# Optimization experiments

Hardware: AMD Instinct MI355X
Metric: run time of the kernel (lower is better)

Reference implementation:

```python
import math
import jax, jax.numpy as jnp
import numpy as np

B, T, C, H, E, K = 2, 2048, 1024, 16, 8, 2
HID = 4 * C
D = C // H

def new_gelu(x):
    return 0.5 * x * (1.0 + jnp.tanh(math.sqrt(2.0 / math.pi) * (x + 0.044715 * x ** 3)))

def layer_norm(x, g, b, eps=1e-5):
    mu = jnp.mean(x, axis=-1, keepdims=True)
    var = jnp.var(x, axis=-1, keepdims=True)
    return (x - mu) / jnp.sqrt(var + eps) * g + b

def setup_inputs():
    key = jax.random.key(0)
    ks = jax.random.split(key, 8)
    s = 0.02
    return {
        'x': jax.random.normal(ks[0], (B, T, C), jnp.float32),
        'ln1_g': jnp.ones((C,), jnp.float32), 'ln1_b': jnp.zeros((C,), jnp.float32),
        'ln2_g': jnp.ones((C,), jnp.float32), 'ln2_b': jnp.zeros((C,), jnp.float32),
        'attn_w': (jax.random.normal(ks[1], (C, 3 * C), jnp.float32) * s),
        'attn_b': jnp.zeros((3 * C,), jnp.float32),
        'proj_w': (jax.random.normal(ks[2], (C, C), jnp.float32) * s),
        'proj_b': jnp.zeros((C,), jnp.float32),
        'router_w': (jax.random.normal(ks[3], (C, E), jnp.float32) * s),
        'fc_w': (jax.random.normal(ks[4], (E, C, HID), jnp.float32) * s),
        'fc_b': jnp.zeros((E, HID), jnp.float32),
        'pj_w': (jax.random.normal(ks[5], (E, HID, C), jnp.float32) * s),
        'pj_b': jnp.zeros((E, C), jnp.float32),
    }

def reference(x, ln1_g, ln1_b, ln2_g, ln2_b, attn_w, attn_b, proj_w, proj_b, router_w, fc_w, fc_b, pj_w, pj_b):
    # --- causal self-attention with residual ---
    h = layer_norm(x, ln1_g, ln1_b)
    qkv = h @ attn_w + attn_b                              # [B,T,3C]
    q, k, v = jnp.split(qkv, 3, axis=-1)
    q = q.reshape(B, T, H, D).transpose(0, 2, 1, 3)        # [B,H,T,D]
    k = k.reshape(B, T, H, D).transpose(0, 2, 1, 3)
    v = v.reshape(B, T, H, D).transpose(0, 2, 1, 3)
    att = jnp.einsum('bhqd,bhkd->bhqk', q, k) * (1.0 / math.sqrt(D))
    mask = jnp.tril(jnp.ones((T, T), dtype=bool))
    att = jnp.where(mask, att, jnp.float32(-jnp.inf))
    att = jax.nn.softmax(att, axis=-1)                     # dropout p=0 (eval)
    y = jnp.einsum('bhqk,bhkd->bhqd', att, v)
    y = y.transpose(0, 2, 1, 3).reshape(B, T, C)
    x = x + (y @ proj_w + proj_b)
    # --- MoE FFN with residual ---
    h2 = layer_norm(x, ln2_g, ln2_b).reshape(B * T, C)     # [N,C]
    logits = h2 @ router_w                                 # [N,E]
    probs = jax.nn.softmax(logits, axis=-1)
    topk_p, topk_i = jax.lax.top_k(probs, K)               # [N,K]
    topk_p = topk_p / jnp.sum(topk_p, axis=-1, keepdims=True)
    # dense combine weights: zero outside selected experts (same math as scatter)
    gate = jnp.zeros((B * T, E), h2.dtype).at[jnp.arange(B * T)[:, None], topk_i].add(topk_p)
    out = jnp.zeros_like(h2)
    for e in range(E):  # fixed small expert loop
        he = new_gelu(h2 @ fc_w[e] + fc_b[e])              # [N,HID]
        out = out + gate[:, e:e + 1] * (he @ pj_w[e] + pj_b[e])
    return x + out.reshape(B, T, C)
```

## Files before the change

### kernel.cpp

```cpp
#include <hip/hip_runtime.h>
#include <math.h>


typedef __bf16 b16v8 __attribute__((ext_vector_type(8)));
typedef float f32x4 __attribute__((ext_vector_type(4)));

#define MFMA(a, b, c) __builtin_amdgcn_mfma_f32_16x16x32_bf16(a, b, c, 0, 0, 0)

#define GLOAD_LDS16(g, l)                                          \
  __builtin_amdgcn_global_load_lds(                                \
      (const __attribute__((address_space(1))) void*)(g),          \
      (__attribute__((address_space(3))) void*)(l), 16, 0, 0)

#define SYNC_VM0()                                       \
  do {                                                   \
    asm volatile("s_waitcnt vmcnt(0)" ::: "memory");     \
    __builtin_amdgcn_s_barrier();                        \
    asm volatile("" ::: "memory");                       \
  } while (0)

constexpr int Bc = 2, Tc = 2048, Cc = 1024, Hc = 16, Dc = 64;
constexpr int Nc = Bc * Tc;
constexpr int HIDc = 4096;
constexpr int Ec = 8;
constexpr int NPAIR = Nc * 2;
constexpr float LOG2E = 1.4426950408889634f;

__device__ inline unsigned short f32_bf16(float f) {
  union { float f; unsigned u; } x; x.f = f;
  unsigned r = x.u + 0x7fffu + ((x.u >> 16) & 1u);
  return (unsigned short)(r >> 16);
}

__device__ inline float gelu_f(float x) {
  float t = 2.3021188f * x * (1.f + 0.044715f * x * x);
  float e = __builtin_amdgcn_exp2f(-t);
  return x * __builtin_amdgcn_rcpf(1.f + e);
}

__global__ __launch_bounds__(256) void convT_kernel(
    const float* __restrict__ src, unsigned short* __restrict__ dst,
    int K, int N) {
  const size_t sb = (size_t)blockIdx.z * K * N;
  const int n0 = blockIdx.x * 32, k0 = blockIdx.y * 32;
  __shared__ float t[32][33];
  const int tx = threadIdx.x & 31, ty = threadIdx.x >> 5;
#pragma unroll
  for (int j = 0; j < 4; ++j)
    t[ty + j * 8][tx] = src[sb + (size_t)(k0 + ty + j * 8) * N + n0 + tx];
  __syncthreads();
#pragma unroll
  for (int j = 0; j < 4; ++j)
    dst[sb + (size_t)(n0 + ty + j * 8) * K + k0 + tx] = f32_bf16(t[tx][ty + j * 8]);
}

__global__ __launch_bounds__(256) void ln1_kernel(
    const float* __restrict__ x, const float* __restrict__ g,
    const float* __restrict__ b, unsigned short* __restrict__ out) {
  const int row = blockIdx.x;
  const int tid = threadIdx.x;
  const float* xr = x + (size_t)row * Cc;
  float v[4]; float s = 0.f, q = 0.f;
#pragma unroll
  for (int j = 0; j < 4; ++j) { v[j] = xr[tid + j * 256]; s += v[j]; q += v[j] * v[j]; }
#pragma unroll
  for (int m = 1; m <= 32; m <<= 1) { s += __shfl_xor(s, m); q += __shfl_xor(q, m); }
  __shared__ float red[2][4];
  const int w = tid >> 6;
  if ((tid & 63) == 0) { red[0][w] = s; red[1][w] = q; }
  __syncthreads();
  s = red[0][0] + red[0][1] + red[0][2] + red[0][3];
  q = red[1][0] + red[1][1] + red[1][2] + red[1][3];
  const float mean = s * (1.f / Cc);
  const float var = q * (1.f / Cc) - mean * mean;
  const float rstd = rsqrtf(var + 1e-5f);
#pragma unroll
  for (int j = 0; j < 4; ++j) {
    int c = tid + j * 256;
    out[(size_t)row * Cc + c] = f32_bf16((v[j] - mean) * rstd * g[c] + b[c]);
  }
}

__global__ __launch_bounds__(256) void ln2_router_kernel(
    const float* __restrict__ x, const float* __restrict__ g,
    const float* __restrict__ b, const float* __restrict__ rw,
    unsigned short* __restrict__ out, int* __restrict__ tki, float* __restrict__ tkp) {
  const int row = blockIdx.x;
  const int tid = threadIdx.x;
  const float* xr = x + (size_t)row * Cc;
  float v[4]; float s = 0.f, q = 0.f;
#pragma unroll
  for (int j = 0; j < 4; ++j) { v[j] = xr[tid + j * 256]; s += v[j]; q += v[j] * v[j]; }
#pragma unroll
  for (int m = 1; m <= 32; m <<= 1) { s += __shfl_xor(s, m); q += __shfl_xor(q, m); }
  __shared__ float red[2][4];
  const int w = tid >> 6;
  if ((tid & 63) == 0) { red[0][w] = s; red[1][w] = q; }
  __syncthreads();
  s = red[0][0] + red[0][1] + red[0][2] + red[0][3];
  q = red[1][0] + red[1][1] + red[1][2] + red[1][3];
  const float mean = s * (1.f / Cc);
  const float var = q * (1.f / Cc) - mean * mean;
  const float rstd = rsqrtf(var + 1e-5f);
  float lg[8] = {0.f, 0.f, 0.f, 0.f, 0.f, 0.f, 0.f, 0.f};
#pragma unroll
  for (int j = 0; j < 4; ++j) {
    int c = tid + j * 256;
    float nv = (v[j] - mean) * rstd * g[c] + b[c];
    out[(size_t)row * Cc + c] = f32_bf16(nv);
    const float* rwc = rw + c * 8;
#pragma unroll
    for (int e = 0; e < 8; ++e) lg[e] += nv * rwc[e];
  }
#pragma unroll
  for (int m = 1; m <= 32; m <<= 1) {
#pragma unroll
    for (int e = 0; e < 8; ++e) lg[e] += __shfl_xor(lg[e], m);
  }
  __shared__ float rl[4][8];
  if ((tid & 63) == 0) {
#pragma unroll
    for (int e = 0; e < 8; ++e) rl[w][e] = lg[e];
  }
  __syncthreads();
  if (tid == 0) {
    float L[8];
#pragma unroll
    for (int e = 0; e < 8; ++e) L[e] = rl[0][e] + rl[1][e] + rl[2][e] + rl[3][e];
    int i1 = 0;
    for (int e = 1; e < 8; ++e) if (L[e] > L[i1]) i1 = e;
    int i2 = (i1 == 0) ? 1 : 0;
    for (int e = 0; e < 8; ++e) if (e != i1 && L[e] > L[i2]) i2 = e;
    float e2 = expf(L[i2] - L[i1]);
    float inv = 1.f / (1.f + e2);
    tki[row * 2] = i1; tki[row * 2 + 1] = i2;
    tkp[row * 2] = inv; tkp[row * 2 + 1] = e2 * inv;
  }
}

__global__ __launch_bounds__(256) void count_kernel(
    const int* __restrict__ tki, int* __restrict__ counts) {
  int n = blockIdx.x * 256 + threadIdx.x;
  if (n >= Nc) return;
  atomicAdd(&counts[tki[n * 2]], 1);
  atomicAdd(&counts[tki[n * 2 + 1]], 1);
}

__global__ void scan_kernel(const int* __restrict__ counts,
                            int* __restrict__ eoff, int* __restrict__ cursor) {
  if (threadIdx.x == 0 && blockIdx.x == 0) {
    int s = 0;
    for (int e = 0; e < Ec; ++e) { eoff[e] = s; cursor[e] = s; s += counts[e]; }
    eoff[Ec] = s;
  }
}

__global__ __launch_bounds__(256) void assign_kernel(
    const int* __restrict__ tki, int* __restrict__ cursor,
    int* __restrict__ slot_tok, int* __restrict__ tok2slot) {
  int n = blockIdx.x * 256 + threadIdx.x;
  if (n >= Nc) return;
#pragma unroll
  for (int kk = 0; kk < 2; ++kk) {
    int e = tki[n * 2 + kk];
    int slot = atomicAdd(&cursor[e], 1);
    slot_tok[slot] = n;
    tok2slot[n * 2 + kk] = slot;
  }
}

struct GArgs {
  const unsigned short* A;
  const unsigned short* Bt;
  const float* bias;
  int M, N, K, lda;
  size_t Bstride; int biasStride;
  const int* eoff;
  const int* slot_tok;
  float* outF;
  const float* resid;
  unsigned short* outB;
  unsigned short* outK;
  unsigned short* outV;
};

template <int MODE>
__global__ __launch_bounds__(256) void gemm128(GArgs g) {
  const int e = blockIdx.z;
  int s0 = 0, Meff = g.M;
  if constexpr (MODE == 2 || MODE == 3) {
    s0 = g.eoff[e];
    Meff = g.eoff[e + 1] - s0;
  }
  const int row0 = blockIdx.y * 128;
  if (row0 >= Meff) return;
  const int col0 = blockIdx.x * 128;

  __shared__ __align__(16) unsigned short As[2][4096];
  __shared__ __align__(16) unsigned short Bs[2][4096];

  const int tid = threadIdx.x;
  const int lane = tid & 63, w = tid >> 6;
  const int wr = w >> 1, wc = w & 1;
  const int fr = lane & 15, fg = lane >> 4;

  const unsigned short* Bt = g.Bt + (size_t)e * g.Bstride;
  const float* bias = g.bias + (size_t)e * g.biasStride;

  size_t aaddr[2], baddr[2];
#pragma unroll
  for (int i = 0; i < 2; ++i) {
    int pos = i * 256 + tid;
    int r = pos >> 2, c8 = (pos & 3) * 8;
    int gr = row0 + r;
    if (gr >= Meff) gr = Meff - 1;
    int srcrow;
    if constexpr (MODE == 2) srcrow = g.slot_tok[s0 + gr];
    else if constexpr (MODE == 3) srcrow = s0 + gr;
    else srcrow = gr;
    aaddr[i] = (size_t)srcrow * g.lda + c8;
    baddr[i] = (size_t)(col0 + r) * g.K + c8;
  }

  auto STAGE = [&](int buf, int k0) {
#pragma unroll
    for (int i = 0; i < 2; ++i) {
      GLOAD_LDS16(g.A + aaddr[i] + k0, &As[buf][i * 2048 + w * 512]);
      GLOAD_LDS16(Bt + baddr[i] + k0, &Bs[buf][i * 2048 + w * 512]);
    }
  };

  f32x4 acc[4][4] = {};
  const int nt = g.K / 32;

  STAGE(0, 0);
  SYNC_VM0();
  int cur = 0;

  for (int t = 0; t < nt; ++t) {
    if (t + 1 < nt) STAGE(cur ^ 1, (t + 1) * 32);
    b16v8 af[4], bfr[4];
#pragma unroll
    for (int mi = 0; mi < 4; ++mi)
      af[mi] = *(const b16v8*)&As[cur][(wr * 64 + mi * 16 + fr) * 32 + fg * 8];
#pragma unroll
    for (int ni = 0; ni < 4; ++ni)
      bfr[ni] = *(const b16v8*)&Bs[cur][(wc * 64 + ni * 16 + fr) * 32 + fg * 8];
#pragma unroll
    for (int mi = 0; mi < 4; ++mi)
#pragma unroll
      for (int ni = 0; ni < 4; ++ni)
        acc[mi][ni] = MFMA(af[mi], bfr[ni], acc[mi][ni]);
    if (t + 1 < nt) {
      SYNC_VM0();
      cur ^= 1;
    }
  }

#pragma unroll
  for (int mi = 0; mi < 4; ++mi) {
#pragma unroll
    for (int ni = 0; ni < 4; ++ni) {
#pragma unroll
      for (int rr = 0; rr < 4; ++rr) {
        int row = row0 + wr * 64 + mi * 16 + fg * 4 + rr;
        int col = col0 + wc * 64 + ni * 16 + fr;
        if (row >= Meff) continue;
        float val = acc[mi][ni][rr] + bias[col];
        if constexpr (MODE == 0) {
          int bb = row >> 11, t = row & (Tc - 1);
          int which = col >> 10, cj = col & (Cc - 1);
          int hd = cj >> 6, d = cj & 63;
          if (which == 0)
            g.outB[(((size_t)(bb * Hc + hd)) * Tc + t) * Dc + d] = f32_bf16(val);
          else if (which == 1)
            g.outK[(((size_t)(bb * Hc + hd)) * Tc + t) * Dc + d] = f32_bf16(val);
          else
            g.outV[(((size_t)(bb * Hc + hd)) * Dc + d) * Tc + t] = f32_bf16(val);
        } else if constexpr (MODE == 1) {
          size_t o = (size_t)row * g.N + col;
          g.outF[o] = val + g.resid[o];
        } else if constexpr (MODE == 2) {
          g.outB[(size_t)(s0 + row) * g.N + col] = f32_bf16(gelu_f(val));
        } else {
          g.outF[(size_t)(s0 + row) * g.N + col] = val;
        }
      }
    }
  }
}

__global__ __launch_bounds__(256) void attn_kernel(
    const unsigned short* __restrict__ q, const unsigned short* __restrict__ k,
    const unsigned short* __restrict__ v, unsigned short* __restrict__ y) {
  const int qt = blockIdx.x, bh = blockIdx.y;
  const int qbase = qt * 64;
  __shared__ __align__(16) unsigned short ldsK[64][72];
  __shared__ __align__(16) unsigned short ldsVT[64][72];
  __shared__ __align__(16) unsigned short ldsP[4][16][72];
  const int tid = threadIdx.x, lane = tid & 63, w = tid >> 6;
  const int fr = lane & 15, fg = lane >> 4;
  const size_t base = (size_t)bh * Tc * Dc;
  const int qrow = qbase + w * 16 + fr;
  b16v8 qa0 = *(const b16v8*)(q + base + (size_t)qrow * Dc + fg * 8);
  b16v8 qa1 = *(const b16v8*)(q + base + (size_t)qrow * Dc + 32 + fg * 8);
  float m[4], lsum[4] = {0.f, 0.f, 0.f, 0.f};
#pragma unroll
  for (int r = 0; r < 4; ++r) m[r] = -3.0e38f;
  f32x4 oacc[4] = {};
  constexpr float SC = 0.125f * LOG2E;

  for (int kb = 0; kb <= qbase; kb += 64) {
    __syncthreads();
#pragma unroll
    for (int i = 0; i < 2; ++i) {
      int pos = i * 256 + tid;
      int r = pos >> 3, cb = (pos & 7) * 8;
      *(uint4*)&ldsK[r][cb]  = *(const uint4*)(k + base + (size_t)(kb + r) * Dc + cb);
      *(uint4*)&ldsVT[r][cb] = *(const uint4*)(v + base + (size_t)r * Tc + kb + cb);
    }
    __syncthreads();

    f32x4 s[4];
#pragma unroll
    for (int ni = 0; ni < 4; ++ni) {
      b16v8 kb0 = *(const b16v8*)&ldsK[ni * 16 + fr][fg * 8];
      b16v8 kb1 = *(const b16v8*)&ldsK[ni * 16 + fr][32 + fg * 8];
      f32x4 z = {};
      z = MFMA(qa0, kb0, z);
      z = MFMA(qa1, kb1, z);
      s[ni] = z;
    }
    const bool diag = (kb == qbase);
#pragma unroll
    for (int ni = 0; ni < 4; ++ni) {
#pragma unroll
      for (int r = 0; r < 4; ++r) {
        float sv = s[ni][r] * SC;
        if (diag) {
          int qr = w * 16 + fg * 4 + r;
          int kc = ni * 16 + fr;
          if (kc > qr) sv = -3.0e38f;
        }
        s[ni][r] = sv;
      }
    }
#pragma unroll
    for (int r = 0; r < 4; ++r) {
      float mx = fmaxf(fmaxf(s[0][r], s[1][r]), fmaxf(s[2][r], s[3][r]));
#pragma unroll
      for (int msk = 1; msk <= 8; msk <<= 1) mx = fmaxf(mx, __shfl_xor(mx, msk));
      float mnew = fmaxf(m[r], mx);
      float alpha = __builtin_amdgcn_exp2f(m[r] - mnew);
      float psum = 0.f;
#pragma unroll
      for (int ni = 0; ni < 4; ++ni) {
        float pp = __builtin_amdgcn_exp2f(s[ni][r] - mnew);
        s[ni][r] = pp;
        psum += pp;
      }
#pragma unroll
      for (int msk = 1; msk <= 8; msk <<= 1) psum += __shfl_xor(psum, msk);
      lsum[r] = lsum[r] * alpha + psum;
      m[r] = mnew;
#pragma unroll
      for (int ni = 0; ni < 4; ++ni) {
        oacc[ni][r] = oacc[ni][r] * alpha;
        ldsP[w][fg * 4 + r][ni * 16 + fr] = f32_bf16(s[ni][r]);
      }
    }
    asm volatile("s_waitcnt lgkmcnt(0)" ::: "memory");
    __builtin_amdgcn_sched_barrier(0);
    b16v8 pa0 = *(const b16v8*)&ldsP[w][fr][fg * 8];
    b16v8 pa1 = *(const b16v8*)&ldsP[w][fr][32 + fg * 8];
#pragma unroll
    for (int ni = 0; ni < 4; ++ni) {
      b16v8 vb0 = *(const b16v8*)&ldsVT[ni * 16 + fr][fg * 8];
      b16v8 vb1 = *(const b16v8*)&ldsVT[ni * 16 + fr][32 + fg * 8];
      oacc[ni] = MFMA(pa0, vb0, oacc[ni]);
      oacc[ni] = MFMA(pa1, vb1, oacc[ni]);
    }
  }

  const int bb = bh >> 4, hh = bh & 15;
#pragma unroll
  for (int r = 0; r < 4; ++r) {
    float rl = __builtin_amdgcn_rcpf(lsum[r]);
#pragma unroll
    for (int ni = 0; ni < 4; ++ni) {
      int t = qbase + w * 16 + fg * 4 + r;
      int d = ni * 16 + fr;
      y[((size_t)(bb * Tc + t)) * Cc + hh * Dc + d] = f32_bf16(oacc[ni][r] * rl);
    }
  }
}

__global__ __launch_bounds__(256) void combine_kernel(
    const float* __restrict__ pair, const float* __restrict__ tkp,
    const int* __restrict__ tok2slot, float* __restrict__ out) {
  const int n = blockIdx.x;
  const int c4 = threadIdx.x * 4;
  const int s0 = tok2slot[n * 2], s1 = tok2slot[n * 2 + 1];
  const float p0 = tkp[n * 2], p1 = tkp[n * 2 + 1];
  float4 a = *(const float4*)&pair[(size_t)s0 * Cc + c4];
  float4 b = *(const float4*)&pair[(size_t)s1 * Cc + c4];
  float4 o = *(float4*)&out[(size_t)n * Cc + c4];
  o.x += p0 * a.x + p1 * b.x;
  o.y += p0 * a.y + p1 * b.y;
  o.z += p0 * a.z + p1 * b.z;
  o.w += p0 * a.w + p1 * b.w;
  *(float4*)&out[(size_t)n * Cc + c4] = o;
}

extern "C" void kernel_launch(void* const* d_in, const int* in_sizes, int n_in,
                              void* d_out, int out_size, void* d_ws, size_t ws_size,
                              hipStream_t stream) {
  const float* x        = (const float*)d_in[0];
  const float* ln1_g    = (const float*)d_in[1];
  const float* ln1_b    = (const float*)d_in[2];
  const float* ln2_g    = (const float*)d_in[3];
  const float* ln2_b    = (const float*)d_in[4];
  const float* attn_w   = (const float*)d_in[5];
  const float* attn_b   = (const float*)d_in[6];
  const float* proj_w   = (const float*)d_in[7];
  const float* proj_b   = (const float*)d_in[8];
  const float* router_w = (const float*)d_in[9];
  const float* fc_w     = (const float*)d_in[10];
  const float* fc_b     = (const float*)d_in[11];
  const float* pj_w     = (const float*)d_in[12];
  const float* pj_b     = (const float*)d_in[13];
  float* out = (float*)d_out;

  char* ws = (char*)d_ws;
  size_t off = 0;
  auto alloc = [&](size_t bytes) -> void* {
    void* p = ws + off;
    off = (off + bytes + 255) & ~(size_t)255;
    return p;
  };
  unsigned short* attn_wT = (unsigned short*)alloc((size_t)3 * Cc * Cc * 2);
  unsigned short* proj_wT = (unsigned short*)alloc((size_t)Cc * Cc * 2);
  unsigned short* fc_wT   = (unsigned short*)alloc((size_t)Ec * HIDc * Cc * 2);
  unsigned short* pj_wT   = (unsigned short*)alloc((size_t)Ec * Cc * HIDc * 2);
  unsigned short* h    = (unsigned short*)alloc((size_t)Nc * Cc * 2);
  unsigned short* qb   = (unsigned short*)alloc((size_t)Nc * Cc * 2);
  unsigned short* kbuf = (unsigned short*)alloc((size_t)Nc * Cc * 2);
  unsigned short* vbuf = (unsigned short*)alloc((size_t)Nc * Cc * 2);
  unsigned short* ybuf = (unsigned short*)alloc((size_t)Nc * Cc * 2);
  unsigned short* he   = (unsigned short*)alloc((size_t)NPAIR * HIDc * 2);
  float* pairout = (float*)alloc((size_t)NPAIR * Cc * 4);
  int*   tki     = (int*)alloc((size_t)Nc * 2 * 4);
  float* tkp     = (float*)alloc((size_t)Nc * 2 * 4);
  int*   counts  = (int*)alloc(Ec * 4);
  int*   eoff    = (int*)alloc((Ec + 1) * 4);
  int*   cursor  = (int*)alloc(Ec * 4);
  int*   slot_tok= (int*)alloc((size_t)NPAIR * 4);
  int*   tok2slot= (int*)alloc((size_t)Nc * 2 * 4);
  (void)ws_size; (void)in_sizes; (void)n_in; (void)out_size;

  convT_kernel<<<dim3(3 * Cc / 32, Cc / 32, 1), 256, 0, stream>>>(attn_w, attn_wT, Cc, 3 * Cc);
  convT_kernel<<<dim3(Cc / 32, Cc / 32, 1), 256, 0, stream>>>(proj_w, proj_wT, Cc, Cc);
  convT_kernel<<<dim3(HIDc / 32, Cc / 32, Ec), 256, 0, stream>>>(fc_w, fc_wT, Cc, HIDc);
  convT_kernel<<<dim3(Cc / 32, HIDc / 32, Ec), 256, 0, stream>>>(pj_w, pj_wT, HIDc, Cc);

  ln1_kernel<<<Nc, 256, 0, stream>>>(x, ln1_g, ln1_b, h);

  {
    GArgs a = {};
    a.A = h; a.Bt = attn_wT; a.bias = attn_b;
    a.M = Nc; a.N = 3 * Cc; a.K = Cc; a.lda = Cc;
    a.outB = qb; a.outK = kbuf; a.outV = vbuf;
    gemm128<0><<<dim3(3 * Cc / 128, Nc / 128, 1), 256, 0, stream>>>(a);
  }

  attn_kernel<<<dim3(Tc / 64, Bc * Hc), 256, 0, stream>>>(qb, kbuf, vbuf, ybuf);

  {
    GArgs p = {};
    p.A = ybuf; p.Bt = proj_wT; p.bias = proj_b;
    p.M = Nc; p.N = Cc; p.K = Cc; p.lda = Cc;
    p.outF = out; p.resid = x;
    gemm128<1><<<dim3(Cc / 128, Nc / 128, 1), 256, 0, stream>>>(p);
  }

  ln2_router_kernel<<<Nc, 256, 0, stream>>>(out, ln2_g, ln2_b, router_w, h, tki, tkp);

  hipMemsetAsync(counts, 0, Ec * sizeof(int), stream);
  count_kernel<<<(Nc + 255) / 256, 256, 0, stream>>>(tki, counts);
  scan_kernel<<<1, 64, 0, stream>>>(counts, eoff, cursor);
  assign_kernel<<<(Nc + 255) / 256, 256, 0, stream>>>(tki, cursor, slot_tok, tok2slot);

  {
    GArgs f = {};
    f.A = h; f.Bt = fc_wT; f.bias = fc_b;
    f.M = Nc; f.N = HIDc; f.K = Cc; f.lda = Cc;
    f.Bstride = (size_t)HIDc * Cc; f.biasStride = HIDc;
    f.eoff = eoff; f.slot_tok = slot_tok;
    f.outB = he;
    gemm128<2><<<dim3(HIDc / 128, Nc / 128, Ec), 256, 0, stream>>>(f);
  }

  {
    GArgs pj = {};
    pj.A = he; pj.Bt = pj_wT; pj.bias = pj_b;
    pj.M = Nc; pj.N = Cc; pj.K = HIDc; pj.lda = HIDc;
    pj.Bstride = (size_t)Cc * HIDc; pj.biasStride = Cc;
    pj.eoff = eoff;
    pj.outF = pairout;
    gemm128<3><<<dim3(Cc / 128, Nc / 128, Ec), 256, 0, stream>>>(pj);
  }

  combine_kernel<<<Nc, 256, 0, stream>>>(pairout, tkp, tok2slot, out);
}
```

Before: 681.7 us.

## Fuse MoE combine into down-proj GEMM via atomics and remap block order

The expert down-projection GEMM now scales each output row by its gate weight and atomically adds it straight into the token's residual output. This removes the fp32 pair-output buffer and the separate combine kernel. Each GEMM also remaps its block index so blocks sharing an expert and column tile run close together, and per-XCD interleaving is applied, with the aim of better weight reuse in cache. The cost is a global float atomic per output element and an order-dependent floating-point sum.

```diff
diff --git a/kernel.cpp b/kernel.cpp
--- a/kernel.cpp
+++ b/kernel.cpp
@@ -156,8 +156,9 @@
 }
 
 __global__ __launch_bounds__(256) void assign_kernel(
-    const int* __restrict__ tki, int* __restrict__ cursor,
-    int* __restrict__ slot_tok, int* __restrict__ tok2slot) {
+    const int* __restrict__ tki, const float* __restrict__ tkp,
+    int* __restrict__ cursor, int* __restrict__ slot_tok,
+    float* __restrict__ slot_gate) {
   int n = blockIdx.x * 256 + threadIdx.x;
   if (n >= Nc) return;
 #pragma unroll
@@ -165,7 +166,7 @@
     int e = tki[n * 2 + kk];
     int slot = atomicAdd(&cursor[e], 1);
     slot_tok[slot] = n;
-    tok2slot[n * 2 + kk] = slot;
+    slot_gate[slot] = tkp[n * 2 + kk];
   }
 }
 
@@ -177,6 +178,7 @@
   size_t Bstride; int biasStride;
   const int* eoff;
   const int* slot_tok;
+  const float* slot_gate;
   float* outF;
   const float* resid;
   unsigned short* outB;
@@ -186,15 +188,23 @@
 
 template <int MODE>
 __global__ __launch_bounds__(256) void gemm128(GArgs g) {
-  const int e = blockIdx.z;
+  const int NCb = gridDim.x, NE = gridDim.z;
+  const int orig = blockIdx.x + NCb * (blockIdx.y + 32 * blockIdx.z);
+  const int chunk = NCb * 4 * NE;
+  const int t_ = (orig & 7) * chunk + (orig >> 3);
+  const int per_e = NCb * 32;
+  const int e = t_ / per_e;
+  const int rem = t_ - e * per_e;
+  const int cb = rem >> 5, rb = rem & 31;
+
   int s0 = 0, Meff = g.M;
   if constexpr (MODE == 2 || MODE == 3) {
     s0 = g.eoff[e];
     Meff = g.eoff[e + 1] - s0;
   }
-  const int row0 = blockIdx.y * 128;
+  const int row0 = rb * 128;
   if (row0 >= Meff) return;
-  const int col0 = blockIdx.x * 128;
+  const int col0 = cb * 128;
 
   __shared__ __align__(16) unsigned short As[2][4096];
   __shared__ __align__(16) unsigned short Bs[2][4096];
@@ -268,22 +278,23 @@
         if (row >= Meff) continue;
         float val = acc[mi][ni][rr] + bias[col];
         if constexpr (MODE == 0) {
-          int bb = row >> 11, t = row & (Tc - 1);
+          int bb = row >> 11, tt = row & (Tc - 1);
           int which = col >> 10, cj = col & (Cc - 1);
           int hd = cj >> 6, d = cj & 63;
           if (which == 0)
-            g.outB[(((size_t)(bb * Hc + hd)) * Tc + t) * Dc + d] = f32_bf16(val);
+            g.outB[(((size_t)(bb * Hc + hd)) * Tc + tt) * Dc + d] = f32_bf16(val);
           else if (which == 1)
-            g.outK[(((size_t)(bb * Hc + hd)) * Tc + t) * Dc + d] = f32_bf16(val);
+            g.outK[(((size_t)(bb * Hc + hd)) * Tc + tt) * Dc + d] = f32_bf16(val);
           else
-            g.outV[(((size_t)(bb * Hc + hd)) * Dc + d) * Tc + t] = f32_bf16(val);
+            g.outV[(((size_t)(bb * Hc + hd)) * Dc + d) * Tc + tt] = f32_bf16(val);
         } else if constexpr (MODE == 1) {
           size_t o = (size_t)row * g.N + col;
           g.outF[o] = val + g.resid[o];
         } else if constexpr (MODE == 2) {
           g.outB[(size_t)(s0 + row) * g.N + col] = f32_bf16(gelu_f(val));
         } else {
-          g.outF[(size_t)(s0 + row) * g.N + col] = val;
+          int tok = g.slot_tok[s0 + row];
+          atomicAdd(&g.outF[(size_t)tok * Cc + col], g.slot_gate[s0 + row] * val);
         }
       }
     }
@@ -393,23 +404,6 @@
       y[((size_t)(bb * Tc + t)) * Cc + hh * Dc + d] = f32_bf16(oacc[ni][r] * rl);
     }
   }
-}
-
-__global__ __launch_bounds__(256) void combine_kernel(
-    const float* __restrict__ pair, const float* __restrict__ tkp,
-    const int* __restrict__ tok2slot, float* __restrict__ out) {
-  const int n = blockIdx.x;
-  const int c4 = threadIdx.x * 4;
-  const int s0 = tok2slot[n * 2], s1 = tok2slot[n * 2 + 1];
-  const float p0 = tkp[n * 2], p1 = tkp[n * 2 + 1];
-  float4 a = *(const float4*)&pair[(size_t)s0 * Cc + c4];
-  float4 b = *(const float4*)&pair[(size_t)s1 * Cc + c4];
-  float4 o = *(float4*)&out[(size_t)n * Cc + c4];
-  o.x += p0 * a.x + p1 * b.x;
-  o.y += p0 * a.y + p1 * b.y;
-  o.z += p0 * a.z + p1 * b.z;
-  o.w += p0 * a.w + p1 * b.w;
-  *(float4*)&out[(size_t)n * Cc + c4] = o;
 }
 
 extern "C" void kernel_launch(void* const* d_in, const int* in_sizes, int n_in,
@@ -448,14 +442,13 @@
   unsigned short* vbuf = (unsigned short*)alloc((size_t)Nc * Cc * 2);
   unsigned short* ybuf = (unsigned short*)alloc((size_t)Nc * Cc * 2);
   unsigned short* he   = (unsigned short*)alloc((size_t)NPAIR * HIDc * 2);
-  float* pairout = (float*)alloc((size_t)NPAIR * Cc * 4);
-  int*   tki     = (int*)alloc((size_t)Nc * 2 * 4);
-  float* tkp     = (float*)alloc((size_t)Nc * 2 * 4);
-  int*   counts  = (int*)alloc(Ec * 4);
-  int*   eoff    = (int*)alloc((Ec + 1) * 4);
-  int*   cursor  = (int*)alloc(Ec * 4);
-  int*   slot_tok= (int*)alloc((size_t)NPAIR * 4);
-  int*   tok2slot= (int*)alloc((size_t)Nc * 2 * 4);
+  int*   tki      = (int*)alloc((size_t)Nc * 2 * 4);
+  float* tkp      = (float*)alloc((size_t)Nc * 2 * 4);
+  int*   counts   = (int*)alloc(Ec * 4);
+  int*   eoff     = (int*)alloc((Ec + 1) * 4);
+  int*   cursor   = (int*)alloc(Ec * 4);
+  int*   slot_tok = (int*)alloc((size_t)NPAIR * 4);
+  float* slot_gate= (float*)alloc((size_t)NPAIR * 4);
   (void)ws_size; (void)in_sizes; (void)n_in; (void)out_size;
 
   convT_kernel<<<dim3(3 * Cc / 32, Cc / 32, 1), 256, 0, stream>>>(attn_w, attn_wT, Cc, 3 * Cc);
@@ -488,7 +481,7 @@
   hipMemsetAsync(counts, 0, Ec * sizeof(int), stream);
   count_kernel<<<(Nc + 255) / 256, 256, 0, stream>>>(tki, counts);
   scan_kernel<<<1, 64, 0, stream>>>(counts, eoff, cursor);
-  assign_kernel<<<(Nc + 255) / 256, 256, 0, stream>>>(tki, cursor, slot_tok, tok2slot);
+  assign_kernel<<<(Nc + 255) / 256, 256, 0, stream>>>(tki, tkp, cursor, slot_tok, slot_gate);
 
   {
     GArgs f = {};
@@ -505,10 +498,8 @@
     pj.A = he; pj.Bt = pj_wT; pj.bias = pj_b;
     pj.M = Nc; pj.N = Cc; pj.K = HIDc; pj.lda = HIDc;
     pj.Bstride = (size_t)Cc * HIDc; pj.biasStride = Cc;
-    pj.eoff = eoff;
-    pj.outF = pairout;
+    pj.eoff = eoff; pj.slot_tok = slot_tok; pj.slot_gate = slot_gate;
+    pj.outF = out;
     gemm128<3><<<dim3(Cc / 128, Nc / 128, Ec), 256, 0, stream>>>(pj);
   }
-
-  combine_kernel<<<Nc, 256, 0, stream>>>(pairout, tkp, tok2slot, out);
-}
+}
```

Result: slower. 731.4 us (+7.3%).
